# Optimization experiments

Measured on AMD Instinct MI355X. Metric: run time of the kernel, lower is better.

Reference implementation:

```python
import jax, jax.numpy as jnp
import numpy as np

# dims
B, HID = 16, 2048            # batch (decode tokens), hidden size
NH, NKV, HD = 16, 8, 128     # q heads, kv heads, head dim (GQA group = 2)
BLK, MAXB = 16, 256          # block size, max blocks per sequence
NBLOCKS = B * MAXB           # total cache blocks (disjoint per sequence)
MAXPOS = 8192
EPS = 1e-6
THETA = 1000000.0
SCALE = HD ** -0.5
Q_SIZE, KV_SIZE = NH * HD, NKV * HD


def _rms(x, w):
    # RMSNorm over last dim (per-head), like NormLayer._normalize
    return x * jax.lax.rsqrt(jnp.mean(x * x, axis=-1, keepdims=True) + EPS) * w


def _rotate(x, cos, sin):
    x1, x2 = jnp.split(x, 2, axis=-1)
    return jnp.concatenate([x1 * cos - x2 * sin, x2 * cos + x1 * sin], axis=-1)


def setup_inputs() -> dict:
    key = jax.random.key(0)
    ks = jax.random.split(key, 8)
    hidden_states = jax.random.normal(ks[0], (B, HID), jnp.float32)
    qkv_w = jax.random.normal(ks[1], (Q_SIZE + 2 * KV_SIZE, HID), jnp.float32) * 0.02
    o_w = jax.random.normal(ks[2], (HID, Q_SIZE), jnp.float32) * 0.02
    q_norm_w = jnp.ones((HD,), jnp.float32)
    k_norm_w = jnp.ones((HD,), jnp.float32)
    k_cache = jax.random.normal(ks[3], (NBLOCKS, BLK, NKV, HD), jnp.float32) * 0.5
    v_cache = jax.random.normal(ks[4], (NBLOCKS, BLK, NKV, HD), jnp.float32) * 0.5
    # disjoint block tables per sequence
    block_tables = jnp.arange(B * MAXB, dtype=jnp.int32).reshape(B, MAXB)
    # context length includes the newly written token (vLLM decode convention)
    context_lens = jax.random.randint(ks[5], (B,), 1, MAXB * BLK + 1).astype(jnp.int32)
    positions = context_lens - 1  # position of the current decode token
    slot_mapping = (block_tables[jnp.arange(B), positions // BLK] * BLK + positions % BLK).astype(jnp.int32)
    # RoPE cache: [max_pos, 1, HD] = cat(cos, sin) over half-dim
    inv_freq = 1.0 / (THETA ** (jnp.arange(0, HD, 2, dtype=jnp.float32) / HD))
    freqs = jnp.arange(MAXPOS, dtype=jnp.float32)[:, None] * inv_freq[None, :]
    cos_sin_cache = jnp.concatenate([jnp.cos(freqs), jnp.sin(freqs)], axis=-1)[:, None, :]
    return dict(hidden_states=hidden_states, positions=positions, qkv_w=qkv_w,
                q_norm_w=q_norm_w, k_norm_w=k_norm_w, o_w=o_w,
                cos_sin_cache=cos_sin_cache, k_cache=k_cache, v_cache=v_cache,
                slot_mapping=slot_mapping, block_tables=block_tables,
                context_lens=context_lens)


def reference(hidden_states, positions, qkv_w, q_norm_w, k_norm_w, o_w,
              cos_sin_cache, k_cache, v_cache, slot_mapping, block_tables,
              context_lens):
    # fused QKV projection (no bias -> QK-norm path)
    qkv = hidden_states @ qkv_w.T
    q, k, v = jnp.split(qkv, [Q_SIZE, Q_SIZE + KV_SIZE], axis=-1)
    q = _rms(q.reshape(B, NH, HD), q_norm_w)
    k = _rms(k.reshape(B, NKV, HD), k_norm_w)
    v = v.reshape(B, NKV, HD)
    # RoPE
    cs = cos_sin_cache[positions]            # [B, 1, HD]
    cos, sin = jnp.split(cs, 2, axis=-1)     # [B, 1, HD/2] each
    q = _rotate(q, cos, sin)
    k = _rotate(k, cos, sin)
    # write new k/v into paged cache at slot_mapping
    D = NKV * HD
    kc = k_cache.reshape(-1, D).at[slot_mapping].set(k.reshape(B, D)).reshape(k_cache.shape)
    vc = v_cache.reshape(-1, D).at[slot_mapping].set(v.reshape(B, D)).reshape(v_cache.shape)
    # paged decode attention: gather blocks, mask by context length
    L = MAXB * BLK
    K = kc[block_tables].reshape(B, L, NKV, HD)
    V = vc[block_tables].reshape(B, L, NKV, HD)
    qg = q.reshape(B, NKV, NH // NKV, HD)    # GQA grouping
    scores = jnp.einsum('bkgd,blkd->bkgl', qg, K) * SCALE
    valid = (jnp.arange(L)[None, :] < context_lens[:, None])[:, None, None, :]
    scores = jnp.where(valid, scores, -jnp.inf)
    p = jax.nn.softmax(scores, axis=-1)
    out = jnp.einsum('bkgl,blkd->bkgd', p, V).reshape(B, Q_SIZE)
    return out @ o_w.T
```

## Files before the change

kernel.cpp:

```cpp
#include <hip/hip_runtime.h>
#include <hip/hip_bf16.h>
#include <cstddef>

#define BATCH    16
#define HID      2048
#define NH       16
#define NKV      8
#define HD       128
#define BLKSZ    16
#define MAXB     256
#define LMAX     4096
#define QSIZE    2048
#define KVSIZE   1024
#define QKVROWS  4096
#define KDIM     2048
#define EPS      1e-6f
#define SCALE    0.08838834764831845f

#define CHUNK    64
#define NCHUNK   64
#define PSTRIDE  130

__global__ __launch_bounds__(256) void gemm_m16(const float* __restrict__ x,
                                                const float* __restrict__ w,
                                                float* __restrict__ out,
                                                int ostride) {
    __shared__ float wt[16][132];
    __shared__ float ht[16][132];
    const int t  = threadIdx.x;
    const int r  = t >> 4;
    const int b  = t & 15;
    const int lr = t >> 4;
    const int c8 = (t & 15) * 8;
    const int row0 = blockIdx.x * 16;

    const float* wl = w + (size_t)(row0 + lr) * KDIM + c8;
    const float* xl = x + (size_t)lr * KDIM + c8;

    float acc = 0.f;
    for (int kc = 0; kc < KDIM; kc += 128) {
        float4 a0 = *(const float4*)(wl + kc);
        float4 a1 = *(const float4*)(wl + kc + 4);
        float4 b0 = *(const float4*)(xl + kc);
        float4 b1 = *(const float4*)(xl + kc + 4);
        __syncthreads();
        *(float4*)&wt[lr][c8]     = a0;
        *(float4*)&wt[lr][c8 + 4] = a1;
        *(float4*)&ht[lr][c8]     = b0;
        *(float4*)&ht[lr][c8 + 4] = b1;
        __syncthreads();
#pragma unroll
        for (int k = 0; k < 128; k += 4) {
            float4 wv = *(const float4*)&wt[r][k];
            float4 hv = *(const float4*)&ht[b][k];
            acc += wv.x * hv.x + wv.y * hv.y + wv.z * hv.z + wv.w * hv.w;
        }
    }
    out[(size_t)b * ostride + row0 + r] = acc;
}

__global__ __launch_bounds__(64) void norm_rope(float* __restrict__ qkv,
                                                const float* __restrict__ qw,
                                                const float* __restrict__ kw,
                                                const float* __restrict__ cs_cache,
                                                const int* __restrict__ positions,
                                                float* __restrict__ k_new,
                                                float* __restrict__ v_new) {
    const int s = blockIdx.x;
    const int b = blockIdx.y;
    const int l = threadIdx.x;
    float* base = qkv + (size_t)b * QKVROWS;

    if (s < NH) {
        float* src = base + s * HD;
        float x1 = src[l], x2 = src[l + 64];
        float ss = x1 * x1 + x2 * x2;
#pragma unroll
        for (int m = 1; m < 64; m <<= 1) ss += __shfl_xor(ss, m, 64);
        float inv = rsqrtf(ss * (1.f / 128.f) + EPS);
        x1 = x1 * inv * qw[l];
        x2 = x2 * inv * qw[l + 64];
        int pos = positions[b];
        float c  = cs_cache[(size_t)pos * HD + l];
        float sn = cs_cache[(size_t)pos * HD + 64 + l];
        src[l]      = (x1 * c - x2 * sn) * SCALE;
        src[l + 64] = (x2 * c + x1 * sn) * SCALE;
    } else if (s < NH + NKV) {
        int h = s - NH;
        const float* src = base + QSIZE + h * HD;
        float x1 = src[l], x2 = src[l + 64];
        float ss = x1 * x1 + x2 * x2;
#pragma unroll
        for (int m = 1; m < 64; m <<= 1) ss += __shfl_xor(ss, m, 64);
        float inv = rsqrtf(ss * (1.f / 128.f) + EPS);
        x1 = x1 * inv * kw[l];
        x2 = x2 * inv * kw[l + 64];
        int pos = positions[b];
        float c  = cs_cache[(size_t)pos * HD + l];
        float sn = cs_cache[(size_t)pos * HD + 64 + l];
        float* dst = k_new + ((size_t)b * NKV + h) * HD;
        dst[l]      = x1 * c - x2 * sn;
        dst[l + 64] = x2 * c + x1 * sn;
    } else {
        int h = s - NH - NKV;
        const float* src = base + QSIZE + KVSIZE + h * HD;
        float* dst = v_new + ((size_t)b * NKV + h) * HD;
        dst[l]      = src[l];
        dst[l + 64] = src[l + 64];
    }
}

__global__ __launch_bounds__(256) void attn_partial(const float* __restrict__ q,
                                                    const float* __restrict__ k_cache,
                                                    const float* __restrict__ v_cache,
                                                    const float* __restrict__ k_new,
                                                    const float* __restrict__ v_new,
                                                    const int* __restrict__ block_tables,
                                                    const int* __restrict__ context_lens,
                                                    float* __restrict__ part) {
    const int b    = blockIdx.z;
    const int kv   = blockIdx.y;
    const int wave = threadIdx.x >> 6;
    const int chunk = blockIdx.x * 4 + wave;
    const int lane = threadIdx.x & 63;
    const int len  = context_lens[b];
    const int start = chunk * CHUNK;
    if (start >= len) return;

    const int t = lane >> 2;
    const int c = lane & 3;

    const float* qb = q + (size_t)b * QKVROWS + (2 * kv) * HD + c * 32;
    float q0[32], q1[32];
#pragma unroll
    for (int j = 0; j < 32; j += 4) {
        *(float4*)&q0[j] = *(const float4*)(qb + j);
        *(float4*)&q1[j] = *(const float4*)(qb + HD + j);
    }

    float acc0[32], acc1[32];
#pragma unroll
    for (int j = 0; j < 32; j++) { acc0[j] = 0.f; acc1[j] = 0.f; }
    float m0 = -1e30f, m1 = -1e30f, l0 = 0.f, l1 = 0.f;

    const int* btab = block_tables + b * MAXB;
    const int nblk = min(CHUNK / BLKSZ, (len - start + BLKSZ - 1) >> 4);

    for (int cb = 0; cb < nblk; cb++) {
        const int gb = (start >> 4) + cb;
        const int pb = btab[gb];
        const float* kp = k_cache + ((size_t)pb * BLKSZ + t) * KVSIZE + kv * HD + c * 32;
        const float* vp = v_cache + ((size_t)pb * BLKSZ + t) * KVSIZE + kv * HD + c * 32;
        float4 kx[8], vx[8];
#pragma unroll
        for (int j = 0; j < 8; j++) kx[j] = ((const float4*)kp)[j];
#pragma unroll
        for (int j = 0; j < 8; j++) vx[j] = ((const float4*)vp)[j];

        const int gidx = start + cb * BLKSZ + t;
        if (gidx == len - 1) {
            const float* kn = k_new + ((size_t)b * NKV + kv) * HD + c * 32;
            const float* vn = v_new + ((size_t)b * NKV + kv) * HD + c * 32;
#pragma unroll
            for (int j = 0; j < 8; j++) {
                kx[j] = ((const float4*)kn)[j];
                vx[j] = ((const float4*)vn)[j];
            }
        }

        float s0 = 0.f, s1 = 0.f;
#pragma unroll
        for (int j = 0; j < 8; j++) {
            const float* kk = (const float*)&kx[j];
#pragma unroll
            for (int e = 0; e < 4; e++) {
                s0 += q0[4 * j + e] * kk[e];
                s1 += q1[4 * j + e] * kk[e];
            }
        }
        s0 += __shfl_xor(s0, 1, 64); s0 += __shfl_xor(s0, 2, 64);
        s1 += __shfl_xor(s1, 1, 64); s1 += __shfl_xor(s1, 2, 64);

        if (gidx >= len) { s0 = -1e30f; s1 = -1e30f; }

        float bm0 = s0, bm1 = s1;
#pragma unroll
        for (int m = 4; m < 64; m <<= 1) {
            bm0 = fmaxf(bm0, __shfl_xor(bm0, m, 64));
            bm1 = fmaxf(bm1, __shfl_xor(bm1, m, 64));
        }
        const float nm0 = fmaxf(m0, bm0), nm1 = fmaxf(m1, bm1);
        const float a0 = __expf(m0 - nm0), a1 = __expf(m1 - nm1);
        const float p0 = __expf(s0 - nm0), p1 = __expf(s1 - nm1);
        m0 = nm0; m1 = nm1;
        l0 = l0 * a0 + p0;
        l1 = l1 * a1 + p1;
#pragma unroll
        for (int j = 0; j < 8; j++) {
            const float* vv = (const float*)&vx[j];
#pragma unroll
            for (int e = 0; e < 4; e++) {
                acc0[4 * j + e] = acc0[4 * j + e] * a0 + p0 * vv[e];
                acc1[4 * j + e] = acc1[4 * j + e] * a1 + p1 * vv[e];
            }
        }
    }

#pragma unroll
    for (int m = 4; m < 64; m <<= 1) {
#pragma unroll
        for (int j = 0; j < 32; j++) {
            acc0[j] += __shfl_xor(acc0[j], m, 64);
            acc1[j] += __shfl_xor(acc1[j], m, 64);
        }
    }
#pragma unroll
    for (int m = 1; m < 64; m <<= 1) {
        l0 += __shfl_xor(l0, m, 64);
        l1 += __shfl_xor(l1, m, 64);
    }
    l0 *= 0.25f; l1 *= 0.25f;

    float* pp0 = part + (size_t)(((b * NKV + kv) * NCHUNK + chunk) * 2 + 0) * PSTRIDE;
    float* pp1 = pp0 + PSTRIDE;
    if (t == 0) {
#pragma unroll
        for (int j = 0; j < 32; j++) {
            pp0[2 + c * 32 + j] = acc0[j];
            pp1[2 + c * 32 + j] = acc1[j];
        }
        if (c == 0) {
            pp0[0] = m0; pp0[1] = l0;
            pp1[0] = m1; pp1[1] = l1;
        }
    }
}

__global__ __launch_bounds__(128) void attn_reduce(const float* __restrict__ part,
                                                   const int* __restrict__ context_lens,
                                                   float* __restrict__ attn_out) {
    const int h = blockIdx.x;
    const int b = blockIdx.y;
    const int d = threadIdx.x;
    const int kv = h >> 1, g = h & 1;
    const int len = context_lens[b];
    const int nch = (len + CHUNK - 1) / CHUNK;

    const float* pb = part + (size_t)(((b * NKV + kv) * NCHUNK) * 2 + g) * PSTRIDE;
    float M = -1e30f;
    for (int i = 0; i < nch; i++) M = fmaxf(M, pb[(size_t)i * 2 * PSTRIDE]);
    float L = 0.f, acc = 0.f;
    for (int i = 0; i < nch; i++) {
        const float* e = pb + (size_t)i * 2 * PSTRIDE;
        float wgt = __expf(e[0] - M);
        L   += wgt * e[1];
        acc += wgt * e[2 + d];
    }
    attn_out[(size_t)b * QSIZE + h * HD + d] = acc / L;
}

extern "C" void kernel_launch(void* const* d_in, const int* in_sizes, int n_in,
                              void* d_out, int out_size, void* d_ws, size_t ws_size,
                              hipStream_t stream) {
    const float* hidden        = (const float*)d_in[0];
    const int*   positions     = (const int*)d_in[1];
    const float* qkv_w         = (const float*)d_in[2];
    const float* q_norm_w      = (const float*)d_in[3];
    const float* k_norm_w      = (const float*)d_in[4];
    const float* o_w           = (const float*)d_in[5];
    const float* cs_cache      = (const float*)d_in[6];
    const float* k_cache       = (const float*)d_in[7];
    const float* v_cache       = (const float*)d_in[8];
    const int*   slot_mapping  = (const int*)d_in[9];
    const int*   block_tables  = (const int*)d_in[10];
    const int*   context_lens  = (const int*)d_in[11];
    float*       out           = (float*)d_out;
    (void)slot_mapping;

    char* ws = (char*)d_ws;
    float* qkv      = (float*)(ws);
    float* attn_out = qkv + (size_t)BATCH * QKVROWS;
    float* part     = attn_out + (size_t)BATCH * QSIZE;
    float* k_new    = part + (size_t)BATCH * NKV * NCHUNK * 2 * PSTRIDE;
    float* v_new    = k_new + (size_t)BATCH * NKV * HD;

    gemm_m16<<<dim3(QKVROWS / 16), 256, 0, stream>>>(hidden, qkv_w, qkv, QKVROWS);
    norm_rope<<<dim3(NH + 2 * NKV, BATCH), 64, 0, stream>>>(
        qkv, q_norm_w, k_norm_w, cs_cache, positions, k_new, v_new);
    attn_partial<<<dim3(NCHUNK / 4, NKV, BATCH), 256, 0, stream>>>(
        qkv, k_cache, v_cache, k_new, v_new, block_tables, context_lens, part);
    attn_reduce<<<dim3(NH, BATCH), 128, 0, stream>>>(part, context_lens, attn_out);
    gemm_m16<<<dim3(HID / 16), 256, 0, stream>>>(attn_out, o_w, out, HID);
}
```

Measured before the change: 620.7 us.

## Split-K QKV GEMM with larger row tiles and register prefetch

The QKV projection becomes a split-K GEMM with 64-row tiles, a 2x2 register microtile per thread, and register double-buffering of the next K slice. Partial sums are written to a workspace and reduced inside norm_rope, which now writes q into a separate buffer. The output projection GEMM gains register prefetch and four-way vector accumulators. The aim is more blocks in flight and more latency hiding while streaming the large weight matrices, at the cost of extra partial-sum traffic and a different summation order.

```diff
diff --git a/kernel.cpp b/kernel.cpp
--- a/kernel.cpp
+++ b/kernel.cpp
@@ -21,59 +21,105 @@
 #define NCHUNK   64
 #define PSTRIDE  130
 
-__global__ __launch_bounds__(256) void gemm_m16(const float* __restrict__ x,
+#define G1_KS    4
+#define G1_KBLK  (KDIM / G1_KS)
+#define G1_NC    (G1_KBLK / 128)
+
+__global__ __launch_bounds__(256) void gemm_qkv(const float* __restrict__ x,
                                                 const float* __restrict__ w,
-                                                float* __restrict__ out,
-                                                int ostride) {
-    __shared__ float wt[16][132];
+                                                float* __restrict__ part) {
+    __shared__ float wt[64][132];
     __shared__ float ht[16][132];
-    const int t  = threadIdx.x;
-    const int r  = t >> 4;
-    const int b  = t & 15;
-    const int lr = t >> 4;
-    const int c8 = (t & 15) * 8;
-    const int row0 = blockIdx.x * 16;
-
-    const float* wl = w + (size_t)(row0 + lr) * KDIM + c8;
-    const float* xl = x + (size_t)lr * KDIM + c8;
-
-    float acc = 0.f;
-    for (int kc = 0; kc < KDIM; kc += 128) {
-        float4 a0 = *(const float4*)(wl + kc);
-        float4 a1 = *(const float4*)(wl + kc + 4);
-        float4 b0 = *(const float4*)(xl + kc);
-        float4 b1 = *(const float4*)(xl + kc + 4);
+    const int tid  = threadIdx.x;
+    const int row0 = blockIdx.x * 64;
+    const int kbase = blockIdx.y * G1_KBLK;
+    const int rt = tid >> 3;
+    const int bt = tid & 7;
+
+    float4 wreg[8], xreg[2];
+#pragma unroll
+    for (int i = 0; i < 8; i++) {
+        int idx = i * 256 + tid, r = idx >> 5, c4 = idx & 31;
+        wreg[i] = *(const float4*)(w + (size_t)(row0 + r) * KDIM + kbase + c4 * 4);
+    }
+#pragma unroll
+    for (int i = 0; i < 2; i++) {
+        int idx = i * 256 + tid, r = idx >> 5, c4 = idx & 31;
+        xreg[i] = *(const float4*)(x + (size_t)r * KDIM + kbase + c4 * 4);
+    }
+
+    float4 a00 = {0.f,0.f,0.f,0.f}, a01 = a00, a10 = a00, a11 = a00;
+
+    for (int c = 0; c < G1_NC; c++) {
+        if (c) __syncthreads();
+#pragma unroll
+        for (int i = 0; i < 8; i++) {
+            int idx = i * 256 + tid, r = idx >> 5, c4 = idx & 31;
+            *(float4*)&wt[r][c4 * 4] = wreg[i];
+        }
+#pragma unroll
+        for (int i = 0; i < 2; i++) {
+            int idx = i * 256 + tid, r = idx >> 5, c4 = idx & 31;
+            *(float4*)&ht[r][c4 * 4] = xreg[i];
+        }
         __syncthreads();
-        *(float4*)&wt[lr][c8]     = a0;
-        *(float4*)&wt[lr][c8 + 4] = a1;
-        *(float4*)&ht[lr][c8]     = b0;
-        *(float4*)&ht[lr][c8 + 4] = b1;
-        __syncthreads();
-#pragma unroll
-        for (int k = 0; k < 128; k += 4) {
-            float4 wv = *(const float4*)&wt[r][k];
-            float4 hv = *(const float4*)&ht[b][k];
-            acc += wv.x * hv.x + wv.y * hv.y + wv.z * hv.z + wv.w * hv.w;
-        }
-    }
-    out[(size_t)b * ostride + row0 + r] = acc;
-}
-
-__global__ __launch_bounds__(64) void norm_rope(float* __restrict__ qkv,
+        if (c + 1 < G1_NC) {
+            const int kc = kbase + (c + 1) * 128;
+#pragma unroll
+            for (int i = 0; i < 8; i++) {
+                int idx = i * 256 + tid, r = idx >> 5, c4 = idx & 31;
+                wreg[i] = *(const float4*)(w + (size_t)(row0 + r) * KDIM + kc + c4 * 4);
+            }
+#pragma unroll
+            for (int i = 0; i < 2; i++) {
+                int idx = i * 256 + tid, r = idx >> 5, c4 = idx & 31;
+                xreg[i] = *(const float4*)(x + (size_t)r * KDIM + kc + c4 * 4);
+            }
+        }
+#pragma unroll
+        for (int k4 = 0; k4 < 32; k4++) {
+            float4 w0 = *(const float4*)&wt[2 * rt][k4 * 4];
+            float4 w1 = *(const float4*)&wt[2 * rt + 1][k4 * 4];
+            float4 x0 = *(const float4*)&ht[2 * bt][k4 * 4];
+            float4 x1 = *(const float4*)&ht[2 * bt + 1][k4 * 4];
+            a00.x += w0.x * x0.x; a00.y += w0.y * x0.y; a00.z += w0.z * x0.z; a00.w += w0.w * x0.w;
+            a01.x += w0.x * x1.x; a01.y += w0.y * x1.y; a01.z += w0.z * x1.z; a01.w += w0.w * x1.w;
+            a10.x += w1.x * x0.x; a10.y += w1.y * x0.y; a10.z += w1.z * x0.z; a10.w += w1.w * x0.w;
+            a11.x += w1.x * x1.x; a11.y += w1.y * x1.y; a11.z += w1.z * x1.z; a11.w += w1.w * x1.w;
+        }
+    }
+    const int r0 = row0 + 2 * rt, r1 = r0 + 1;
+    const int b0 = 2 * bt, b1 = b0 + 1;
+    const size_t kb = (size_t)blockIdx.y * 16;
+    part[(kb + b0) * QKVROWS + r0] = (a00.x + a00.y) + (a00.z + a00.w);
+    part[(kb + b1) * QKVROWS + r0] = (a01.x + a01.y) + (a01.z + a01.w);
+    part[(kb + b0) * QKVROWS + r1] = (a10.x + a10.y) + (a10.z + a10.w);
+    part[(kb + b1) * QKVROWS + r1] = (a11.x + a11.y) + (a11.z + a11.w);
+}
+
+__device__ __forceinline__ float qkv_sum(const float* __restrict__ part, int b, int col) {
+    float s = 0.f;
+#pragma unroll
+    for (int ks = 0; ks < G1_KS; ks++)
+        s += part[((size_t)(ks * 16 + b)) * QKVROWS + col];
+    return s;
+}
+
+__global__ __launch_bounds__(64) void norm_rope(const float* __restrict__ part,
                                                 const float* __restrict__ qw,
                                                 const float* __restrict__ kw,
                                                 const float* __restrict__ cs_cache,
                                                 const int* __restrict__ positions,
+                                                float* __restrict__ q_buf,
                                                 float* __restrict__ k_new,
                                                 float* __restrict__ v_new) {
     const int s = blockIdx.x;
     const int b = blockIdx.y;
     const int l = threadIdx.x;
-    float* base = qkv + (size_t)b * QKVROWS;
 
     if (s < NH) {
-        float* src = base + s * HD;
-        float x1 = src[l], x2 = src[l + 64];
+        float x1 = qkv_sum(part, b, s * HD + l);
+        float x2 = qkv_sum(part, b, s * HD + l + 64);
         float ss = x1 * x1 + x2 * x2;
 #pragma unroll
         for (int m = 1; m < 64; m <<= 1) ss += __shfl_xor(ss, m, 64);
@@ -83,12 +129,13 @@
         int pos = positions[b];
         float c  = cs_cache[(size_t)pos * HD + l];
         float sn = cs_cache[(size_t)pos * HD + 64 + l];
-        src[l]      = (x1 * c - x2 * sn) * SCALE;
-        src[l + 64] = (x2 * c + x1 * sn) * SCALE;
+        float* dst = q_buf + (size_t)b * QSIZE + s * HD;
+        dst[l]      = (x1 * c - x2 * sn) * SCALE;
+        dst[l + 64] = (x2 * c + x1 * sn) * SCALE;
     } else if (s < NH + NKV) {
         int h = s - NH;
-        const float* src = base + QSIZE + h * HD;
-        float x1 = src[l], x2 = src[l + 64];
+        float x1 = qkv_sum(part, b, QSIZE + h * HD + l);
+        float x2 = qkv_sum(part, b, QSIZE + h * HD + l + 64);
         float ss = x1 * x1 + x2 * x2;
 #pragma unroll
         for (int m = 1; m < 64; m <<= 1) ss += __shfl_xor(ss, m, 64);
@@ -103,10 +150,9 @@
         dst[l + 64] = x2 * c + x1 * sn;
     } else {
         int h = s - NH - NKV;
-        const float* src = base + QSIZE + KVSIZE + h * HD;
         float* dst = v_new + ((size_t)b * NKV + h) * HD;
-        dst[l]      = src[l];
-        dst[l + 64] = src[l + 64];
+        dst[l]      = qkv_sum(part, b, QSIZE + KVSIZE + h * HD + l);
+        dst[l + 64] = qkv_sum(part, b, QSIZE + KVSIZE + h * HD + l + 64);
     }
 }
 
@@ -130,7 +176,7 @@
     const int t = lane >> 2;
     const int c = lane & 3;
 
-    const float* qb = q + (size_t)b * QKVROWS + (2 * kv) * HD + c * 32;
+    const float* qb = q + (size_t)b * QSIZE + (2 * kv) * HD + c * 32;
     float q0[32], q1[32];
 #pragma unroll
     for (int j = 0; j < 32; j += 4) {
@@ -257,6 +303,52 @@
         acc += wgt * e[2 + d];
     }
     attn_out[(size_t)b * QSIZE + h * HD + d] = acc / L;
+}
+
+__global__ __launch_bounds__(256) void gemm_m16(const float* __restrict__ x,
+                                                const float* __restrict__ w,
+                                                float* __restrict__ out,
+                                                int ostride) {
+    __shared__ float wt[16][132];
+    __shared__ float ht[16][132];
+    const int t  = threadIdx.x;
+    const int r  = t >> 4;
+    const int b  = t & 15;
+    const int lr = t >> 4;
+    const int c8 = (t & 15) * 8;
+    const int row0 = blockIdx.x * 16;
+
+    const float* wl = w + (size_t)(row0 + lr) * KDIM + c8;
+    const float* xl = x + (size_t)lr * KDIM + c8;
+
+    float4 a0 = *(const float4*)(wl);
+    float4 a1 = *(const float4*)(wl + 4);
+    float4 b0 = *(const float4*)(xl);
+    float4 b1 = *(const float4*)(xl + 4);
+
+    float4 av = {0.f, 0.f, 0.f, 0.f};
+    for (int kc = 0; kc < KDIM; kc += 128) {
+        if (kc) __syncthreads();
+        *(float4*)&wt[lr][c8]     = a0;
+        *(float4*)&wt[lr][c8 + 4] = a1;
+        *(float4*)&ht[lr][c8]     = b0;
+        *(float4*)&ht[lr][c8 + 4] = b1;
+        __syncthreads();
+        if (kc + 128 < KDIM) {
+            a0 = *(const float4*)(wl + kc + 128);
+            a1 = *(const float4*)(wl + kc + 132);
+            b0 = *(const float4*)(xl + kc + 128);
+            b1 = *(const float4*)(xl + kc + 132);
+        }
+#pragma unroll
+        for (int k = 0; k < 128; k += 4) {
+            float4 wv = *(const float4*)&wt[r][k];
+            float4 hv = *(const float4*)&ht[b][k];
+            av.x += wv.x * hv.x; av.y += wv.y * hv.y;
+            av.z += wv.z * hv.z; av.w += wv.w * hv.w;
+        }
+    }
+    out[(size_t)b * ostride + row0 + r] = (av.x + av.y) + (av.z + av.w);
 }
 
 extern "C" void kernel_launch(void* const* d_in, const int* in_sizes, int n_in,
@@ -277,18 +369,19 @@
     float*       out           = (float*)d_out;
     (void)slot_mapping;
 
-    char* ws = (char*)d_ws;
-    float* qkv      = (float*)(ws);
-    float* attn_out = qkv + (size_t)BATCH * QKVROWS;
+    float* ws       = (float*)d_ws;
+    float* qkv_part = ws;
+    float* q_buf    = qkv_part + (size_t)G1_KS * 16 * QKVROWS;
+    float* attn_out = q_buf + (size_t)BATCH * QSIZE;
     float* part     = attn_out + (size_t)BATCH * QSIZE;
     float* k_new    = part + (size_t)BATCH * NKV * NCHUNK * 2 * PSTRIDE;
     float* v_new    = k_new + (size_t)BATCH * NKV * HD;
 
-    gemm_m16<<<dim3(QKVROWS / 16), 256, 0, stream>>>(hidden, qkv_w, qkv, QKVROWS);
+    gemm_qkv<<<dim3(QKVROWS / 64, G1_KS), 256, 0, stream>>>(hidden, qkv_w, qkv_part);
     norm_rope<<<dim3(NH + 2 * NKV, BATCH), 64, 0, stream>>>(
-        qkv, q_norm_w, k_norm_w, cs_cache, positions, k_new, v_new);
+        qkv_part, q_norm_w, k_norm_w, cs_cache, positions, q_buf, k_new, v_new);
     attn_partial<<<dim3(NCHUNK / 4, NKV, BATCH), 256, 0, stream>>>(
-        qkv, k_cache, v_cache, k_new, v_new, block_tables, context_lens, part);
+        q_buf, k_cache, v_cache, k_new, v_new, block_tables, context_lens, part);
     attn_reduce<<<dim3(NH, BATCH), 128, 0, stream>>>(part, context_lens, attn_out);
     gemm_m16<<<dim3(HID / 16), 256, 0, stream>>>(attn_out, o_w, out, HID);
 }
```

New measurement: 615.1 us. Within noise of the previous version (-0.9%).
